# Kernel tuning notes

Hardware: AMD Instinct MI355X
Metric: run time of the kernel (lower is better)

The kernel has to match this reference:

```python
import jax, jax.numpy as jnp
import numpy as np

EPS = 1e-5
B, L, DM, DI, DR, DS, K = 1, 1024, 2048, 4096, 128, 16, 3
DT_MAX, DT_MIN, DT_FLOOR = 0.1, 0.001, 1e-4


def setup_inputs() -> dict:
    key = jax.random.key(0)
    ks = jax.random.split(key, 10)
    sc = lambda k, sh, s=0.02: (jax.random.normal(k, sh, jnp.float32) * s)
    # dt_proj bias init (softplus-inverse of dt sampled log-uniform in [dt_min, dt_max])
    dt = jnp.exp(jax.random.uniform(ks[7], (DI,), jnp.float32)
                 * (np.log(DT_MAX) - np.log(DT_MIN)) + np.log(DT_MIN))
    dt = jnp.clip(dt, DT_FLOOR, None)
    inv_dt = dt + jnp.log(-jnp.expm1(-dt))
    dt_std = DR ** (-0.5)  # dt_rank**-0.5 * dt_scale
    return {
        "x": jax.random.normal(ks[0], (B, L, DM), jnp.float32),
        "h": jnp.zeros((B, L, DI, DS), jnp.float32),
        "norm_w": jnp.ones((DM,), jnp.float32),
        "in_proj_w": sc(ks[1], (2 * DI, DM)),
        "conv_w": sc(ks[2], (DI, 1, K), 0.1),      # depthwise: (out=DI, in/groups=1, K)
        "conv_b": jnp.zeros((DI,), jnp.float32),
        "x_proj_w": sc(ks[3], (DR + 2 * DS, DI)),
        "dt_proj_w": jax.random.uniform(ks[4], (DI, DR), jnp.float32, -dt_std, dt_std),
        "dt_proj_b": inv_dt,
        "A_log": jnp.log(jnp.tile(jnp.arange(1, DS + 1, dtype=jnp.float32), (DI, 1))),
        "D": jnp.ones((DI,), jnp.float32),
        "out_proj_w": sc(ks[5], (DM, DI)),
    }


def reference(x, h, norm_w, in_proj_w, conv_w, conv_b, x_proj_w,
              dt_proj_w, dt_proj_b, A_log, D, out_proj_w):
    # RMSNorm
    xn = x * jax.lax.rsqrt(jnp.mean(x * x, axis=-1, keepdims=True) + EPS) * norm_w
    # in_proj -> split into x-branch and gate z
    xz = xn @ in_proj_w.T                      # (B,L,2*DI)
    xs, z = xz[..., :DI], xz[..., DI:]
    # depthwise conv over sequence (padding preserves L for odd K)
    xc = jax.lax.conv_general_dilated(
        jnp.transpose(xs, (0, 2, 1)), conv_w, (1,), [((K - 1) // 2, (K - 1) // 2)],
        dimension_numbers=("NCH", "OIH", "NCH"), feature_group_count=DI)
    xc = jnp.transpose(xc, (0, 2, 1)) + conv_b  # (B,L,DI)
    xc = jax.nn.silu(xc)
    # ssm_step (elementwise over L; h is per-position state)
    A = -jnp.exp(A_log)                        # (DI,DS)
    dBC = xc @ x_proj_w.T                      # (B,L,DR+2*DS)
    delta = jax.nn.softplus(dBC[..., :DR] @ dt_proj_w.T + dt_proj_b)  # (B,L,DI)
    Bm = dBC[..., DR:DR + DS]                  # (B,L,DS)
    Cm = dBC[..., DR + DS:]                    # (B,L,DS)
    deltaA = jnp.exp(delta[..., None] * A)     # (B,L,DI,DS)
    BX = delta[..., None] * Bm[:, :, None, :] * xc[..., None]  # (B,L,DI,DS)
    h_new = deltaA * h + BX                    # (B,L,DI,DS)
    y = jnp.einsum("blds,bls->bld", h_new, Cm) + D * xc
    out = (y * jax.nn.silu(z)) @ out_proj_w.T + xn  # residual adds normed x
    return out, h_new
```

## Files before the change

kernel.cpp:

```cpp
#include <hip/hip_runtime.h>
#include <hip/hip_bf16.h>
#include <math.h>

#define L_   1024
#define DM_  2048
#define DI_  4096
#define DR_  128
#define DS_  16
#define DBC_ 160

typedef __attribute__((ext_vector_type(4))) float f32x4;
typedef __attribute__((ext_vector_type(8))) short s16x8;

__device__ inline unsigned short f2b(float f) {
  unsigned int u = __float_as_uint(f);
  u += 0x7fffu + ((u >> 16) & 1u);
  return (unsigned short)(u >> 16);
}
__device__ inline float b2f(unsigned short u) {
  return __uint_as_float(((unsigned int)u) << 16);
}

__device__ inline void gload_lds16(const void* g, void* l) {
  __builtin_amdgcn_global_load_lds(
      (const __attribute__((address_space(1))) void*)g,
      (__attribute__((address_space(3))) void*)l, 16, 0, 0);
}

__launch_bounds__(256)
__global__ void rms_convert_kernel(const float* __restrict__ x, const float* __restrict__ w,
                                   float* __restrict__ xn, unsigned short* __restrict__ xnb,
                                   const float* __restrict__ w_in, const float* __restrict__ w_out,
                                   const float* __restrict__ w_dt, const float* __restrict__ w_xp,
                                   unsigned short* __restrict__ wib, unsigned short* __restrict__ wob,
                                   unsigned short* __restrict__ dtwb, unsigned short* __restrict__ xpwb) {
  if (blockIdx.x < L_) {
    int l = blockIdx.x;
    const float4* xr = (const float4*)(x + (size_t)l * DM_);
    const float4* wr = (const float4*)w;
    float4 v0 = xr[threadIdx.x];
    float4 v1 = xr[threadIdx.x + 256];
    float ss = v0.x*v0.x + v0.y*v0.y + v0.z*v0.z + v0.w*v0.w
             + v1.x*v1.x + v1.y*v1.y + v1.z*v1.z + v1.w*v1.w;
    for (int off = 32; off > 0; off >>= 1) ss += __shfl_down(ss, off, 64);
    __shared__ float sbuf[4];
    int lane = threadIdx.x & 63, wid = threadIdx.x >> 6;
    if (lane == 0) sbuf[wid] = ss;
    __syncthreads();
    float tot = sbuf[0] + sbuf[1] + sbuf[2] + sbuf[3];
    float scale = rsqrtf(tot / (float)DM_ + 1e-5f);
    float4 w0 = wr[threadIdx.x], w1 = wr[threadIdx.x + 256];
    float4 o0, o1;
    o0.x = v0.x * scale * w0.x; o0.y = v0.y * scale * w0.y;
    o0.z = v0.z * scale * w0.z; o0.w = v0.w * scale * w0.w;
    o1.x = v1.x * scale * w1.x; o1.y = v1.y * scale * w1.y;
    o1.z = v1.z * scale * w1.z; o1.w = v1.w * scale * w1.w;
    float4* outr = (float4*)(xn + (size_t)l * DM_);
    outr[threadIdx.x] = o0;
    outr[threadIdx.x + 256] = o1;
    uint2 p0, p1;
    p0.x = (unsigned)f2b(o0.x) | ((unsigned)f2b(o0.y) << 16);
    p0.y = (unsigned)f2b(o0.z) | ((unsigned)f2b(o0.w) << 16);
    p1.x = (unsigned)f2b(o1.x) | ((unsigned)f2b(o1.y) << 16);
    p1.y = (unsigned)f2b(o1.z) | ((unsigned)f2b(o1.w) << 16);
    uint2* ob = (uint2*)(xnb + (size_t)l * DM_);
    ob[threadIdx.x] = p0;
    ob[threadIdx.x + 256] = p1;
    return;
  }
  const int N1 = 2 * DI_ * DM_ / 4;
  const int N2 = DM_ * DI_ / 4;
  const int N3 = DI_ * DR_ / 4;
  const int N4 = DBC_ * DI_ / 4;
  int i = (blockIdx.x - L_) * 256 + threadIdx.x;
  const float* src; unsigned short* dst; int off;
  if (i < N1)                { src = w_in;  dst = wib;  off = i; }
  else if (i < N1 + N2)      { src = w_out; dst = wob;  off = i - N1; }
  else if (i < N1 + N2 + N3) { src = w_dt;  dst = dtwb; off = i - N1 - N2; }
  else if (i < N1 + N2 + N3 + N4) { src = w_xp; dst = xpwb; off = i - N1 - N2 - N3; }
  else return;
  float4 v = ((const float4*)src)[off];
  uint2 p;
  p.x = (unsigned)f2b(v.x) | ((unsigned)f2b(v.y) << 16);
  p.y = (unsigned)f2b(v.z) | ((unsigned)f2b(v.w) << 16);
  ((uint2*)dst)[off] = p;
}

template<int EPI>
__launch_bounds__(256)
__global__ void gemm_bf16_mfma(const unsigned short* __restrict__ A,
                               const unsigned short* __restrict__ W,
                               void* __restrict__ Cv_, int M, int N, int K,
                               const float* __restrict__ aux) {
  __shared__ unsigned short As[2][128 * 32];
  __shared__ unsigned short Ws[2][128 * 32];
  int nwg = gridDim.x * gridDim.y;
  int flat = blockIdx.y * gridDim.x + blockIdx.x;
  int q8 = nwg >> 3;
  int swz = (flat & 7) * q8 + (flat >> 3);
  int bxi = swz % gridDim.x, byi = swz / gridDim.x;
  int bm = byi * 128, bn = bxi * 128;
  int tid = threadIdx.x;
  int w = tid >> 6, lane = tid & 63;
  int wr = (w >> 1) * 64, wc = (w & 1) * 64;
  int ch0 = w * 64 + lane, ch1 = (4 + w) * 64 + lane;
  int row0 = ch0 >> 2, kc0 = ch0 & 3;
  int row1 = ch1 >> 2, kc1 = ch1 & 3;

  f32x4 acc[4][4];
#pragma unroll
  for (int m = 0; m < 4; m++)
#pragma unroll
    for (int n = 0; n < 4; n++) acc[m][n] = (f32x4){0.f, 0.f, 0.f, 0.f};

  int kb = lane >> 4, r = lane & 15;

#define STAGE_(buf, k0)                                                          \
  do {                                                                           \
    gload_lds16(A + (size_t)(bm + row0) * K + (k0) + kc0 * 8, &As[buf][ch0 * 8]);\
    gload_lds16(W + (size_t)(bn + row0) * K + (k0) + kc0 * 8, &Ws[buf][ch0 * 8]);\
    gload_lds16(A + (size_t)(bm + row1) * K + (k0) + kc1 * 8, &As[buf][ch1 * 8]);\
    gload_lds16(W + (size_t)(bn + row1) * K + (k0) + kc1 * 8, &Ws[buf][ch1 * 8]);\
  } while (0)

  STAGE_(0, 0);
  __syncthreads();
  int nt = K >> 5;
  for (int t = 0; t < nt; t++) {
    int cur = t & 1;
    if (t + 1 < nt) STAGE_(cur ^ 1, (t + 1) * 32);
    s16x8 a[4], b[4];
#pragma unroll
    for (int m = 0; m < 4; m++)
      a[m] = *(const s16x8*)(&As[cur][(wr + m * 16 + r) * 32 + kb * 8]);
#pragma unroll
    for (int n = 0; n < 4; n++)
      b[n] = *(const s16x8*)(&Ws[cur][(wc + n * 16 + r) * 32 + kb * 8]);
#pragma unroll
    for (int m = 0; m < 4; m++)
#pragma unroll
      for (int n = 0; n < 4; n++)
        acc[m][n] = __builtin_amdgcn_mfma_f32_16x16x32_bf16(a[m], b[n], acc[m][n], 0, 0, 0);
    __syncthreads();
  }
#undef STAGE_
  int q = lane >> 4;
#pragma unroll
  for (int m = 0; m < 4; m++) {
#pragma unroll
    for (int n = 0; n < 4; n++) {
#pragma unroll
      for (int j = 0; j < 4; j++) {
        int row = bm + wr + m * 16 + q * 4 + j;
        int col = bn + wc + n * 16 + r;
        float v = acc[m][n][j];
        if (EPI == 1) {
          v += aux[col];
          v = fmaxf(v, 0.f) + log1pf(__expf(-fabsf(v)));
          ((unsigned short*)Cv_)[(size_t)row * N + col] = f2b(v);
        }
        if (EPI == 3) {
          ((unsigned short*)Cv_)[(size_t)row * N + col] = f2b(v);
        }
      }
    }
  }
}

__launch_bounds__(256)
__global__ void gemm_bf16_mfma_bm64(const unsigned short* __restrict__ A,
                                    const unsigned short* __restrict__ W,
                                    float* __restrict__ C, int M, int N, int K,
                                    const float* __restrict__ aux) {
  __shared__ unsigned short As[2][64 * 32];
  __shared__ unsigned short Ws[2][128 * 32];
  int nwg = gridDim.x * gridDim.y;
  int flat = blockIdx.y * gridDim.x + blockIdx.x;
  int q8 = nwg >> 3;
  int swz = (flat & 7) * q8 + (flat >> 3);
  int bxi = swz % gridDim.x, byi = swz / gridDim.x;
  int bm = byi * 64, bn = bxi * 128;
  int tid = threadIdx.x;
  int w = tid >> 6, lane = tid & 63;
  int wr = (w >> 1) * 32, wc = (w & 1) * 64;
  int chA = w * 64 + lane;
  int rowA = chA >> 2, kcA = chA & 3;
  int ch0 = w * 64 + lane, ch1 = (4 + w) * 64 + lane;
  int row0 = ch0 >> 2, kc0 = ch0 & 3;
  int row1 = ch1 >> 2, kc1 = ch1 & 3;
  f32x4 acc[2][4];
#pragma unroll
  for (int m = 0; m < 2; m++)
#pragma unroll
    for (int n = 0; n < 4; n++) acc[m][n] = (f32x4){0.f, 0.f, 0.f, 0.f};

  int kb = lane >> 4, r = lane & 15;

#define STAGE_(buf, k0)                                                          \
  do {                                                                           \
    gload_lds16(A + (size_t)(bm + rowA) * K + (k0) + kcA * 8, &As[buf][chA * 8]);\
    gload_lds16(W + (size_t)(bn + row0) * K + (k0) + kc0 * 8, &Ws[buf][ch0 * 8]);\
    gload_lds16(W + (size_t)(bn + row1) * K + (k0) + kc1 * 8, &Ws[buf][ch1 * 8]);\
  } while (0)

  STAGE_(0, 0);
  __syncthreads();
  int nt = K >> 5;
  for (int t = 0; t < nt; t++) {
    int cur = t & 1;
    if (t + 1 < nt) STAGE_(cur ^ 1, (t + 1) * 32);
    s16x8 a[2], b[4];
#pragma unroll
    for (int m = 0; m < 2; m++)
      a[m] = *(const s16x8*)(&As[cur][(wr + m * 16 + r) * 32 + kb * 8]);
#pragma unroll
    for (int n = 0; n < 4; n++)
      b[n] = *(const s16x8*)(&Ws[cur][(wc + n * 16 + r) * 32 + kb * 8]);
#pragma unroll
    for (int m = 0; m < 2; m++)
#pragma unroll
      for (int n = 0; n < 4; n++)
        acc[m][n] = __builtin_amdgcn_mfma_f32_16x16x32_bf16(a[m], b[n], acc[m][n], 0, 0, 0);
    __syncthreads();
  }
#undef STAGE_
  int q = lane >> 4;
#pragma unroll
  for (int m = 0; m < 2; m++) {
#pragma unroll
    for (int n = 0; n < 4; n++) {
#pragma unroll
      for (int j = 0; j < 4; j++) {
        int row = bm + wr + m * 16 + q * 4 + j;
        int col = bn + wc + n * 16 + r;
        C[(size_t)row * N + col] = acc[m][n][j] + aux[(size_t)row * N + col];
      }
    }
  }
}

__launch_bounds__(256)
__global__ void conv_silu_kernel(const unsigned short* __restrict__ xzb, const float* __restrict__ cw,
                                 const float* __restrict__ cb, unsigned short* __restrict__ xcb) {
  int idx = blockIdx.x * 256 + threadIdx.x;
  int l = idx >> 12, d = idx & (DI_ - 1);
  float w0 = cw[d * 3 + 0], w1 = cw[d * 3 + 1], w2 = cw[d * 3 + 2];
  float acc = cb[d];
  const unsigned short* base = xzb + d;
  if (l > 0)      acc = fmaf(w0, b2f(base[(size_t)(l - 1) * (2 * DI_)]), acc);
  acc = fmaf(w1, b2f(base[(size_t)l * (2 * DI_)]), acc);
  if (l < L_ - 1) acc = fmaf(w2, b2f(base[(size_t)(l + 1) * (2 * DI_)]), acc);
  float sig = 1.f / (1.f + __expf(-acc));
  xcb[idx] = f2b(acc * sig);
}

__launch_bounds__(256)
__global__ void xproj_stage1_mfma(const unsigned short* __restrict__ xcb,
                                  const unsigned short* __restrict__ Wb,
                                  float* __restrict__ part) {
  __shared__ unsigned short As[2][64 * 32];
  __shared__ unsigned short Bs[2][160 * 32];
  int sp = blockIdx.x;
  int l0 = blockIdx.y * 64;
  int tid = threadIdx.x, w = tid >> 6, lane = tid & 63;
  int wr = (w >> 1) * 32, wc = (w & 1) * 80;
  int kb = lane >> 4, r = lane & 15;
  int chA = w * 64 + lane;
  int rowA = chA >> 2, kcA = chA & 3;
  f32x4 acc[2][5];
#pragma unroll
  for (int m = 0; m < 2; m++)
#pragma unroll
    for (int n = 0; n < 5; n++) acc[m][n] = (f32x4){0.f, 0.f, 0.f, 0.f};

#define STAGE_(buf, k0)                                                            \
  do {                                                                             \
    gload_lds16(xcb + (size_t)(l0 + rowA) * DI_ + (k0) + kcA * 8, &As[buf][chA * 8]);\
    _Pragma("unroll")                                                              \
    for (int i = 0; i < 3; i++) {                                                  \
      int g = i * 4 + w;                                                           \
      if (g < 10) {                                                                \
        int ch = g * 64 + lane;                                                    \
        int row = ch >> 2, kc = ch & 3;                                            \
        gload_lds16(Wb + (size_t)row * DI_ + (k0) + kc * 8, &Bs[buf][ch * 8]);     \
      }                                                                            \
    }                                                                              \
  } while (0)

  int kbase = sp * 256;
  STAGE_(0, kbase);
  __syncthreads();
  for (int kt = 0; kt < 8; kt++) {
    int cur = kt & 1;
    if (kt + 1 < 8) STAGE_(cur ^ 1, kbase + (kt + 1) * 32);
    s16x8 a[2], b[5];
#pragma unroll
    for (int m = 0; m < 2; m++)
      a[m] = *(const s16x8*)(&As[cur][(wr + m * 16 + r) * 32 + kb * 8]);
#pragma unroll
    for (int n = 0; n < 5; n++)
      b[n] = *(const s16x8*)(&Bs[cur][(wc + n * 16 + r) * 32 + kb * 8]);
#pragma unroll
    for (int m = 0; m < 2; m++)
#pragma unroll
      for (int n = 0; n < 5; n++)
        acc[m][n] = __builtin_amdgcn_mfma_f32_16x16x32_bf16(a[m], b[n], acc[m][n], 0, 0, 0);
    __syncthreads();
  }
#undef STAGE_
  int q = lane >> 4;
  float* pb = part + (size_t)sp * (L_ * DBC_) + (size_t)l0 * DBC_;
#pragma unroll
  for (int m = 0; m < 2; m++)
#pragma unroll
    for (int n = 0; n < 5; n++)
#pragma unroll
      for (int j = 0; j < 4; j++)
        pb[(size_t)(wr + m * 16 + q * 4 + j) * DBC_ + wc + n * 16 + r] = acc[m][n][j];
}

__launch_bounds__(256)
__global__ void xproj_stage2(const float* __restrict__ part, float* __restrict__ dBC,
                             unsigned short* __restrict__ dtb) {
  int i = blockIdx.x * 256 + threadIdx.x;
  float s = 0.f;
#pragma unroll
  for (int sp = 0; sp < 16; sp++) s += part[(size_t)sp * (L_ * DBC_) + i];
  dBC[i] = s;
  int l = i / DBC_, col = i - l * DBC_;
  if (col < DR_) dtb[(size_t)l * DR_ + col] = f2b(s);
}

__launch_bounds__(256)
__global__ void ssm_kernel2(const unsigned short* __restrict__ xzb, const unsigned short* __restrict__ xcb,
                            const float* __restrict__ dBC, const unsigned short* __restrict__ deltab,
                            const float* __restrict__ h, const float* __restrict__ A_log,
                            const float* __restrict__ Dp, float* __restrict__ h_out,
                            unsigned short* __restrict__ yzb) {
  int pair = threadIdx.x >> 2;
  int q = threadIdx.x & 3;
  for (int base = blockIdx.x * 64; base < L_ * DI_; base += gridDim.x * 64) {
    int idx = base + pair;
    int l = idx >> 12, d = idx & (DI_ - 1);
    float dv = b2f(deltab[idx]);
    float xv = b2f(xcb[idx]);
    float4 hv = *(const float4*)(h + (size_t)idx * DS_ + q * 4);
    float4 Al = *(const float4*)(A_log + (size_t)d * DS_ + q * 4);
    float4 Bv = *(const float4*)(dBC + (size_t)l * DBC_ + DR_ + q * 4);
    float4 Cv = *(const float4*)(dBC + (size_t)l * DBC_ + DR_ + DS_ + q * 4);
    float4 hn;
    hn.x = __expf(dv * -__expf(Al.x)) * hv.x + dv * Bv.x * xv;
    hn.y = __expf(dv * -__expf(Al.y)) * hv.y + dv * Bv.y * xv;
    hn.z = __expf(dv * -__expf(Al.z)) * hv.z + dv * Bv.z * xv;
    hn.w = __expf(dv * -__expf(Al.w)) * hv.w + dv * Bv.w * xv;
    *(float4*)(h_out + (size_t)idx * DS_ + q * 4) = hn;
    float y = hn.x * Cv.x + hn.y * Cv.y + hn.z * Cv.z + hn.w * Cv.w;
    y += __shfl_xor(y, 1, 64);
    y += __shfl_xor(y, 2, 64);
    if (q == 0) {
      y = fmaf(Dp[d], xv, y);
      float zv = b2f(xzb[(size_t)l * (2 * DI_) + DI_ + d]);
      float sig = 1.f / (1.f + __expf(-zv));
      yzb[idx] = f2b(y * zv * sig);
    }
  }
}

extern "C" void kernel_launch(void* const* d_in, const int* in_sizes, int n_in,
                              void* d_out, int out_size, void* d_ws, size_t ws_size,
                              hipStream_t stream) {
  const float* x         = (const float*)d_in[0];
  const float* h         = (const float*)d_in[1];
  const float* norm_w    = (const float*)d_in[2];
  const float* in_proj_w = (const float*)d_in[3];
  const float* conv_w    = (const float*)d_in[4];
  const float* conv_b    = (const float*)d_in[5];
  const float* x_proj_w  = (const float*)d_in[6];
  const float* dt_proj_w = (const float*)d_in[7];
  const float* dt_proj_b = (const float*)d_in[8];
  const float* A_log     = (const float*)d_in[9];
  const float* Dvec      = (const float*)d_in[10];
  const float* out_projw = (const float*)d_in[11];

  float* out   = (float*)d_out;
  float* h_out = out + (size_t)L_ * DM_;

  float* ws    = (float*)d_ws;
  float* xn    = ws;
  float* dBC   = xn    + (size_t)L_ * DM_;
  float* part  = dBC   + (size_t)L_ * DBC_;
  unsigned short* xnb   = (unsigned short*)(part + (size_t)16 * L_ * DBC_);
  unsigned short* wib   = xnb   + (size_t)L_ * DM_;
  unsigned short* wob   = wib   + (size_t)2 * DI_ * DM_;
  unsigned short* yzb   = wob   + (size_t)DM_ * DI_;
  unsigned short* dtb   = yzb   + (size_t)L_ * DI_;
  unsigned short* dtwb  = dtb   + (size_t)L_ * DR_;
  unsigned short* xpwb  = dtwb  + (size_t)DI_ * DR_;
  unsigned short* xcb   = xpwb  + (size_t)DBC_ * DI_;
  unsigned short* xzb   = xcb   + (size_t)L_ * DI_;
  unsigned short* deltab= xzb   + (size_t)L_ * 2 * DI_;

  const int CONV_BLKS = (2 * DI_ * DM_ + DM_ * DI_ + DI_ * DR_ + DBC_ * DI_) / 4 / 256;
  rms_convert_kernel<<<L_ + CONV_BLKS, 256, 0, stream>>>(
      x, norm_w, xn, xnb, in_proj_w, out_projw, dt_proj_w, x_proj_w, wib, wob, dtwb, xpwb);
  gemm_bf16_mfma<3><<<dim3(2 * DI_ / 128, L_ / 128), 256, 0, stream>>>(
      xnb, wib, xzb, L_, 2 * DI_, DM_, nullptr);
  conv_silu_kernel<<<L_ * DI_ / 256, 256, 0, stream>>>(xzb, conv_w, conv_b, xcb);
  xproj_stage1_mfma<<<dim3(16, 16), 256, 0, stream>>>(xcb, xpwb, part);
  xproj_stage2<<<L_ * DBC_ / 256, 256, 0, stream>>>(part, dBC, dtb);
  gemm_bf16_mfma<1><<<dim3(DI_ / 128, L_ / 128), 256, 0, stream>>>(
      dtb, dtwb, deltab, L_, DI_, DR_, dt_proj_b);
  ssm_kernel2<<<4096, 256, 0, stream>>>(
      xzb, xcb, dBC, deltab, h, A_log, Dvec, h_out, yzb);
  gemm_bf16_mfma_bm64<<<dim3(DM_ / 128, L_ / 64), 256, 0, stream>>>(
      yzb, wob, out, L_, DM_, DI_, xn);
}
```

Before: 322.4 us.

## Fuse dt_proj into SSM kernel and use bf16 normed residual

Removes the separate dt_proj MFMA GEMM along with its bf16 activation, weight and delta buffers. Each SSM thread group now computes the 128-long dt dot product in fp32 from dBC and the fp32 dt_proj weights, then applies the bias and softplus inline. The fp32 normed-x buffer is dropped as well, and the out-projection epilogue reads the residual from the bf16 copy. This cuts a kernel launch and several intermediate global round trips, but adds a lot of per-element vector FMA work and cache traffic inside the memory-bound SSM kernel, and lowers the residual's precision.

```diff
diff --git a/kernel.cpp b/kernel.cpp
--- a/kernel.cpp
+++ b/kernel.cpp
@@ -29,11 +29,11 @@
 
 __launch_bounds__(256)
 __global__ void rms_convert_kernel(const float* __restrict__ x, const float* __restrict__ w,
-                                   float* __restrict__ xn, unsigned short* __restrict__ xnb,
+                                   unsigned short* __restrict__ xnb,
                                    const float* __restrict__ w_in, const float* __restrict__ w_out,
-                                   const float* __restrict__ w_dt, const float* __restrict__ w_xp,
+                                   const float* __restrict__ w_xp,
                                    unsigned short* __restrict__ wib, unsigned short* __restrict__ wob,
-                                   unsigned short* __restrict__ dtwb, unsigned short* __restrict__ xpwb) {
+                                   unsigned short* __restrict__ xpwb) {
   if (blockIdx.x < L_) {
     int l = blockIdx.x;
     const float4* xr = (const float4*)(x + (size_t)l * DM_);
@@ -55,9 +55,6 @@
     o0.z = v0.z * scale * w0.z; o0.w = v0.w * scale * w0.w;
     o1.x = v1.x * scale * w1.x; o1.y = v1.y * scale * w1.y;
     o1.z = v1.z * scale * w1.z; o1.w = v1.w * scale * w1.w;
-    float4* outr = (float4*)(xn + (size_t)l * DM_);
-    outr[threadIdx.x] = o0;
-    outr[threadIdx.x + 256] = o1;
     uint2 p0, p1;
     p0.x = (unsigned)f2b(o0.x) | ((unsigned)f2b(o0.y) << 16);
     p0.y = (unsigned)f2b(o0.z) | ((unsigned)f2b(o0.w) << 16);
@@ -70,14 +67,12 @@
   }
   const int N1 = 2 * DI_ * DM_ / 4;
   const int N2 = DM_ * DI_ / 4;
-  const int N3 = DI_ * DR_ / 4;
   const int N4 = DBC_ * DI_ / 4;
   int i = (blockIdx.x - L_) * 256 + threadIdx.x;
   const float* src; unsigned short* dst; int off;
   if (i < N1)                { src = w_in;  dst = wib;  off = i; }
   else if (i < N1 + N2)      { src = w_out; dst = wob;  off = i - N1; }
-  else if (i < N1 + N2 + N3) { src = w_dt;  dst = dtwb; off = i - N1 - N2; }
-  else if (i < N1 + N2 + N3 + N4) { src = w_xp; dst = xpwb; off = i - N1 - N2 - N3; }
+  else if (i < N1 + N2 + N4) { src = w_xp;  dst = xpwb; off = i - N1 - N2; }
   else return;
   float4 v = ((const float4*)src)[off];
   uint2 p;
@@ -154,11 +149,6 @@
         int row = bm + wr + m * 16 + q * 4 + j;
         int col = bn + wc + n * 16 + r;
         float v = acc[m][n][j];
-        if (EPI == 1) {
-          v += aux[col];
-          v = fmaxf(v, 0.f) + log1pf(__expf(-fabsf(v)));
-          ((unsigned short*)Cv_)[(size_t)row * N + col] = f2b(v);
-        }
         if (EPI == 3) {
           ((unsigned short*)Cv_)[(size_t)row * N + col] = f2b(v);
         }
@@ -171,7 +161,7 @@
 __global__ void gemm_bf16_mfma_bm64(const unsigned short* __restrict__ A,
                                     const unsigned short* __restrict__ W,
                                     float* __restrict__ C, int M, int N, int K,
-                                    const float* __restrict__ aux) {
+                                    const unsigned short* __restrict__ auxb) {
   __shared__ unsigned short As[2][64 * 32];
   __shared__ unsigned short Ws[2][128 * 32];
   int nwg = gridDim.x * gridDim.y;
@@ -233,7 +223,7 @@
       for (int j = 0; j < 4; j++) {
         int row = bm + wr + m * 16 + q * 4 + j;
         int col = bn + wc + n * 16 + r;
-        C[(size_t)row * N + col] = acc[m][n][j] + aux[(size_t)row * N + col];
+        C[(size_t)row * N + col] = acc[m][n][j] + b2f(auxb[(size_t)row * N + col]);
       }
     }
   }
@@ -320,20 +310,18 @@
 }
 
 __launch_bounds__(256)
-__global__ void xproj_stage2(const float* __restrict__ part, float* __restrict__ dBC,
-                             unsigned short* __restrict__ dtb) {
+__global__ void xproj_stage2(const float* __restrict__ part, float* __restrict__ dBC) {
   int i = blockIdx.x * 256 + threadIdx.x;
   float s = 0.f;
 #pragma unroll
   for (int sp = 0; sp < 16; sp++) s += part[(size_t)sp * (L_ * DBC_) + i];
   dBC[i] = s;
-  int l = i / DBC_, col = i - l * DBC_;
-  if (col < DR_) dtb[(size_t)l * DR_ + col] = f2b(s);
-}
-
-__launch_bounds__(256)
-__global__ void ssm_kernel2(const unsigned short* __restrict__ xzb, const unsigned short* __restrict__ xcb,
-                            const float* __restrict__ dBC, const unsigned short* __restrict__ deltab,
+}
+
+__launch_bounds__(256)
+__global__ void ssm_kernel3(const unsigned short* __restrict__ xzb, const unsigned short* __restrict__ xcb,
+                            const float* __restrict__ dBC, const float* __restrict__ dtw,
+                            const float* __restrict__ dt_b,
                             const float* __restrict__ h, const float* __restrict__ A_log,
                             const float* __restrict__ Dp, float* __restrict__ h_out,
                             unsigned short* __restrict__ yzb) {
@@ -342,7 +330,20 @@
   for (int base = blockIdx.x * 64; base < L_ * DI_; base += gridDim.x * 64) {
     int idx = base + pair;
     int l = idx >> 12, d = idx & (DI_ - 1);
-    float dv = b2f(deltab[idx]);
+    const float* dbc_l = dBC + (size_t)l * DBC_ + q * 32;
+    const float* wrow  = dtw + (size_t)d * DR_ + q * 32;
+    float s = 0.f;
+#pragma unroll
+    for (int i = 0; i < 8; i++) {
+      float4 a4 = *(const float4*)(dbc_l + i * 4);
+      float4 w4 = *(const float4*)(wrow + i * 4);
+      s = fmaf(a4.x, w4.x, s); s = fmaf(a4.y, w4.y, s);
+      s = fmaf(a4.z, w4.z, s); s = fmaf(a4.w, w4.w, s);
+    }
+    s += __shfl_xor(s, 1, 64);
+    s += __shfl_xor(s, 2, 64);
+    float tt = s + dt_b[d];
+    float dv = fmaxf(tt, 0.f) + log1pf(__expf(-fabsf(tt)));
     float xv = b2f(xcb[idx]);
     float4 hv = *(const float4*)(h + (size_t)idx * DS_ + q * 4);
     float4 Al = *(const float4*)(A_log + (size_t)d * DS_ + q * 4);
@@ -386,32 +387,26 @@
   float* h_out = out + (size_t)L_ * DM_;
 
   float* ws    = (float*)d_ws;
-  float* xn    = ws;
-  float* dBC   = xn    + (size_t)L_ * DM_;
+  float* dBC   = ws;
   float* part  = dBC   + (size_t)L_ * DBC_;
   unsigned short* xnb   = (unsigned short*)(part + (size_t)16 * L_ * DBC_);
   unsigned short* wib   = xnb   + (size_t)L_ * DM_;
   unsigned short* wob   = wib   + (size_t)2 * DI_ * DM_;
   unsigned short* yzb   = wob   + (size_t)DM_ * DI_;
-  unsigned short* dtb   = yzb   + (size_t)L_ * DI_;
-  unsigned short* dtwb  = dtb   + (size_t)L_ * DR_;
-  unsigned short* xpwb  = dtwb  + (size_t)DI_ * DR_;
+  unsigned short* xpwb  = yzb   + (size_t)L_ * DI_;
   unsigned short* xcb   = xpwb  + (size_t)DBC_ * DI_;
   unsigned short* xzb   = xcb   + (size_t)L_ * DI_;
-  unsigned short* deltab= xzb   + (size_t)L_ * 2 * DI_;
-
-  const int CONV_BLKS = (2 * DI_ * DM_ + DM_ * DI_ + DI_ * DR_ + DBC_ * DI_) / 4 / 256;
+
+  const int CONV_BLKS = (2 * DI_ * DM_ + DM_ * DI_ + DBC_ * DI_) / 4 / 256;
   rms_convert_kernel<<<L_ + CONV_BLKS, 256, 0, stream>>>(
-      x, norm_w, xn, xnb, in_proj_w, out_projw, dt_proj_w, x_proj_w, wib, wob, dtwb, xpwb);
+      x, norm_w, xnb, in_proj_w, out_projw, x_proj_w, wib, wob, xpwb);
   gemm_bf16_mfma<3><<<dim3(2 * DI_ / 128, L_ / 128), 256, 0, stream>>>(
       xnb, wib, xzb, L_, 2 * DI_, DM_, nullptr);
   conv_silu_kernel<<<L_ * DI_ / 256, 256, 0, stream>>>(xzb, conv_w, conv_b, xcb);
   xproj_stage1_mfma<<<dim3(16, 16), 256, 0, stream>>>(xcb, xpwb, part);
-  xproj_stage2<<<L_ * DBC_ / 256, 256, 0, stream>>>(part, dBC, dtb);
-  gemm_bf16_mfma<1><<<dim3(DI_ / 128, L_ / 128), 256, 0, stream>>>(
-      dtb, dtwb, deltab, L_, DI_, DR_, dt_proj_b);
-  ssm_kernel2<<<4096, 256, 0, stream>>>(
-      xzb, xcb, dBC, deltab, h, A_log, Dvec, h_out, yzb);
+  xproj_stage2<<<L_ * DBC_ / 256, 256, 0, stream>>>(part, dBC);
+  ssm_kernel3<<<4096, 256, 0, stream>>>(
+      xzb, xcb, dBC, dt_proj_w, dt_proj_b, h, A_log, Dvec, h_out, yzb);
   gemm_bf16_mfma_bm64<<<dim3(DM_ / 128, L_ / 64), 256, 0, stream>>>(
-      yzb, wob, out, L_, DM_, DI_, xn);
-}
+      yzb, wob, out, L_, DM_, DI_, xnb);
+}
```

Measured after the change: 754.8 us. +134.1%, slower.
